# Kernel optimization log

Measured on AMD Instinct MI355X. Metric: run time of the kernel, lower is better.

Reference implementation:

```python
import jax, jax.numpy as jnp
import numpy as np

QMIN, QMAX = -128, 127  # int8 range


def _quantize(x, scale, zero_point):
    """Affine quantize float -> int8: clamp(round(x/scale) + zp, -128, 127)."""
    q = jnp.round(x / scale) + zero_point
    return jnp.clip(q, QMIN, QMAX).astype(jnp.int8)


def setup_inputs() -> dict:
    key = jax.random.key(0)
    k1, k2, k3 = jax.random.split(key, 3)
    N, IN, OUT = 8192, 4096, 4096
    inp = jax.random.normal(k1, (N, IN), dtype=jnp.float32)
    # int8 weight table [OUT, IN]
    weight = jax.random.randint(k2, (OUT, IN), QMIN, QMAX + 1, dtype=jnp.int32).astype(jnp.int8)
    # int32 bias [OUT]
    bias = jax.random.randint(k3, (OUT,), -(2 ** 15), 2 ** 15, dtype=jnp.int32)
    return {
        "input": inp,
        "weight": weight,
        "bias": bias,
        "input_scale": 0.02,
        "input_zero_point": 0,
        "output_scale": 4096.0,
        "output_zero_point": 0,
    }


def reference(input, weight, bias, input_scale, input_zero_point, output_scale, output_zero_point):
    # 1) affine quantize input to int8
    q_input = _quantize(input, input_scale, input_zero_point)
    # 2) int32 matmul: F.linear(q_input.int32, weight.int32, bias.int32)
    acc = jnp.matmul(q_input.astype(jnp.int32), weight.astype(jnp.int32).T) + bias  # [N, OUT] int32
    # 3) requantize int32 accumulator to int8 with output scale/zero-point
    q_output = _quantize(acc.astype(jnp.float32), output_scale, output_zero_point)
    return q_output
```

## Files before the change

kernel.cpp:

```cpp
#include <hip/hip_runtime.h>
#include <stdint.h>

typedef int v4i __attribute__((ext_vector_type(4)));

__device__ __forceinline__ int clamp_i8(int v) {
    return v < -128 ? -128 : (v > 127 ? 127 : v);
}

__device__ __forceinline__ void async_load16(const void* g, void* l) {
    __builtin_amdgcn_global_load_lds(
        (const __attribute__((address_space(1))) void*)g,
        (__attribute__((address_space(3))) void*)l, 16, 0, 0);
}

__global__ void quant_input_kernel(const float* __restrict__ x, int8_t* __restrict__ q,
                                   const float* __restrict__ scale_p,
                                   const int* __restrict__ zp_p, int n4) {
    int t = blockIdx.x * blockDim.x + threadIdx.x;
    if (t >= n4) return;
    const float s = *scale_p;
    const int zp = *zp_p;
    float4 v = ((const float4*)x)[t];
    int q0 = clamp_i8((int)rintf(v.x / s) + zp);
    int q1 = clamp_i8((int)rintf(v.y / s) + zp);
    int q2 = clamp_i8((int)rintf(v.z / s) + zp);
    int q3 = clamp_i8((int)rintf(v.w / s) + zp);
    int packed = (q0 & 255) | ((q1 & 255) << 8) | ((q2 & 255) << 16) | ((q3 & 255) << 24);
    ((int*)q)[t] = packed;
}

__global__ void pack_weight_kernel(const int* __restrict__ w, int8_t* __restrict__ q, int n4) {
    int t = blockIdx.x * blockDim.x + threadIdx.x;
    if (t >= n4) return;
    int4 v = ((const int4*)w)[t];
    int packed = (v.x & 255) | ((v.y & 255) << 8) | ((v.z & 255) << 16) | ((v.w & 255) << 24);
    ((int*)q)[t] = packed;
}

#define BM 128
#define BN 128
#define BK 64

__global__ __launch_bounds__(256) void gemm_i8_kernel(
    const int8_t* __restrict__ A, const int8_t* __restrict__ W,
    const int* __restrict__ bias, int* __restrict__ C,
    const float* __restrict__ oscale_p, const int* __restrict__ ozp_p,
    int N, int K, int M) {
    __shared__ int8_t lA[BM * BK];
    __shared__ int8_t lW[BN * BK];

    const int tid = threadIdx.x;
    const int lane = tid & 63;
    const int w = tid >> 6;
    const int wm = w & 1;
    const int wn = w >> 1;
    const int qm = lane & 15;
    const int qk = lane >> 4;

    const int bm = blockIdx.y * BM;
    const int bn = blockIdx.x * BN;

    const int s_row = w * 32 + (lane >> 2);
    const int s_col = (lane & 3) * 16;
    const int8_t* gA = A + (int64_t)(bm + s_row) * K + s_col;
    const int8_t* gW = W + (int64_t)(bn + s_row) * K + s_col;
    int8_t* lA0 = &lA[w * 2048];
    int8_t* lW0 = &lW[w * 2048];
    const int64_t rowskip = (int64_t)16 * K;

    v4i acc[4][4];
#pragma unroll
    for (int i = 0; i < 4; i++)
#pragma unroll
        for (int j = 0; j < 4; j++) acc[i][j] = (v4i){0, 0, 0, 0};

    for (int kt = 0; kt < K; kt += BK) {
        async_load16(gA + kt, lA0);
        async_load16(gA + kt + rowskip, lA0 + 1024);
        async_load16(gW + kt, lW0);
        async_load16(gW + kt + rowskip, lW0 + 1024);
        __syncthreads();

        v4i af[4], bf[4];
#pragma unroll
        for (int ms = 0; ms < 4; ms++)
            af[ms] = *(const v4i*)&lA[(wm * 64 + ms * 16 + qm) * BK + qk * 16];
#pragma unroll
        for (int ns = 0; ns < 4; ns++)
            bf[ns] = *(const v4i*)&lW[(wn * 64 + ns * 16 + qm) * BK + qk * 16];

#pragma unroll
        for (int ms = 0; ms < 4; ms++)
#pragma unroll
            for (int ns = 0; ns < 4; ns++)
                acc[ms][ns] = __builtin_amdgcn_mfma_i32_16x16x64_i8(af[ms], bf[ns],
                                                                    acc[ms][ns], 0, 0, 0);
        __syncthreads();
    }

    const float os = *oscale_p;
    const int ozp = *ozp_p;
#pragma unroll
    for (int ns = 0; ns < 4; ns++) {
        const int gn = bn + wn * 64 + ns * 16 + qm;
        const int bv = bias[gn];
#pragma unroll
        for (int ms = 0; ms < 4; ms++) {
            const int gm = bm + wm * 64 + ms * 16 + qk * 4;
            v4i a = acc[ms][ns];
#pragma unroll
            for (int r = 0; r < 4; r++) {
                int v = a[r] + bv;
                int q = (int)rintf((float)v / os) + ozp;
                q = clamp_i8(q);
                C[(int64_t)(gm + r) * M + gn] = q;
            }
        }
    }
}

extern "C" void kernel_launch(void* const* d_in, const int* in_sizes, int n_in,
                              void* d_out, int out_size, void* d_ws, size_t ws_size,
                              hipStream_t stream) {
    const float* x = (const float*)d_in[0];
    const int* wgt = (const int*)d_in[1];
    const int* bias = (const int*)d_in[2];
    const float* in_scale = (const float*)d_in[3];
    const int* in_zp = (const int*)d_in[4];
    const float* out_scale = (const float*)d_in[5];
    const int* out_zp = (const int*)d_in[6];

    const int64_t x_elems = (int64_t)in_sizes[0];
    const int OUT = in_sizes[2];
    const int K = in_sizes[1] / OUT;
    const int N = (int)(x_elems / K);

    int8_t* qA = (int8_t*)d_ws;
    int8_t* qW = qA + x_elems;

    {
        int n4 = (int)(x_elems / 4);
        quant_input_kernel<<<(n4 + 255) / 256, 256, 0, stream>>>(x, qA, in_scale, in_zp, n4);
    }
    {
        int n4 = (int)(((int64_t)OUT * K) / 4);
        pack_weight_kernel<<<(n4 + 255) / 256, 256, 0, stream>>>(wgt, qW, n4);
    }
    dim3 grid(OUT / BN, N / BM);
    gemm_i8_kernel<<<grid, 256, 0, stream>>>(qA, qW, bias, (int*)d_out,
                                             out_scale, out_zp, N, K, OUT);
}
```

Before: 443.2 us.

## Enlarge GEMM tile to 256x128 and switch to 32x32x32 int8 MFMA

Doubles the M tile to 256 rows and has each wave compute a 128x64 sub-tile with 32x32x32 int8 MFMAs over two k-steps per 64-wide K tile. This raises arithmetic intensity per LDS and global load and cuts the number of instructions per FLOP. The epilogue and the input quantizer now multiply by a precomputed reciprocal instead of dividing, which can change rounding in rare edge cases. LDS use grows to 24KB per block, and launch bounds now ask for two blocks per CU.

New measurement: 427.8 us. 3.5% less time.

```diff
diff --git a/kernel.cpp b/kernel.cpp
--- a/kernel.cpp
+++ b/kernel.cpp
@@ -2,6 +2,7 @@
 #include <stdint.h>
 
 typedef int v4i __attribute__((ext_vector_type(4)));
+typedef int v16i __attribute__((ext_vector_type(16)));
 
 __device__ __forceinline__ int clamp_i8(int v) {
     return v < -128 ? -128 : (v > 127 ? 127 : v);
@@ -18,13 +19,13 @@
                                    const int* __restrict__ zp_p, int n4) {
     int t = blockIdx.x * blockDim.x + threadIdx.x;
     if (t >= n4) return;
-    const float s = *scale_p;
+    const float inv = 1.0f / *scale_p;
     const int zp = *zp_p;
     float4 v = ((const float4*)x)[t];
-    int q0 = clamp_i8((int)rintf(v.x / s) + zp);
-    int q1 = clamp_i8((int)rintf(v.y / s) + zp);
-    int q2 = clamp_i8((int)rintf(v.z / s) + zp);
-    int q3 = clamp_i8((int)rintf(v.w / s) + zp);
+    int q0 = clamp_i8((int)rintf(v.x * inv) + zp);
+    int q1 = clamp_i8((int)rintf(v.y * inv) + zp);
+    int q2 = clamp_i8((int)rintf(v.z * inv) + zp);
+    int q3 = clamp_i8((int)rintf(v.w * inv) + zp);
     int packed = (q0 & 255) | ((q1 & 255) << 8) | ((q2 & 255) << 16) | ((q3 & 255) << 24);
     ((int*)q)[t] = packed;
 }
@@ -37,83 +38,95 @@
     ((int*)q)[t] = packed;
 }
 
-#define BM 128
+#define BM 256
 #define BN 128
 #define BK 64
 
-__global__ __launch_bounds__(256) void gemm_i8_kernel(
+__global__ __launch_bounds__(256, 2) void gemm_i8_kernel(
     const int8_t* __restrict__ A, const int8_t* __restrict__ W,
     const int* __restrict__ bias, int* __restrict__ C,
     const float* __restrict__ oscale_p, const int* __restrict__ ozp_p,
     int N, int K, int M) {
     __shared__ int8_t lA[BM * BK];
-    __shared__ int8_t lW[BN * BK];
+    __shared__ int8_t lB[BN * BK];
 
     const int tid = threadIdx.x;
     const int lane = tid & 63;
     const int w = tid >> 6;
-    const int wm = w & 1;
-    const int wn = w >> 1;
-    const int qm = lane & 15;
-    const int qk = lane >> 4;
+    const int wm = w >> 1;
+    const int wn = w & 1;
 
     const int bm = blockIdx.y * BM;
     const int bn = blockIdx.x * BN;
 
-    const int s_row = w * 32 + (lane >> 2);
+    const int s_sub = lane >> 2;
     const int s_col = (lane & 3) * 16;
-    const int8_t* gA = A + (int64_t)(bm + s_row) * K + s_col;
-    const int8_t* gW = W + (int64_t)(bn + s_row) * K + s_col;
-    int8_t* lA0 = &lA[w * 2048];
-    int8_t* lW0 = &lW[w * 2048];
-    const int64_t rowskip = (int64_t)16 * K;
+    const int8_t* gA = A + (int64_t)(bm + w * 64 + s_sub) * K + s_col;
+    const int8_t* gB = W + (int64_t)(bn + w * 32 + s_sub) * K + s_col;
+    int8_t* lA0 = &lA[w * 4096];
+    int8_t* lB0 = &lB[w * 2048];
+    const int64_t rs = (int64_t)16 * K;
 
-    v4i acc[4][4];
+    const int m0 = lane & 31;
+    const int kh = (lane >> 5) * 16;
+
+    v16i acc[4][2];
 #pragma unroll
     for (int i = 0; i < 4; i++)
 #pragma unroll
-        for (int j = 0; j < 4; j++) acc[i][j] = (v4i){0, 0, 0, 0};
+        for (int j = 0; j < 2; j++)
+#pragma unroll
+            for (int r = 0; r < 16; r++) acc[i][j][r] = 0;
 
     for (int kt = 0; kt < K; kt += BK) {
-        async_load16(gA + kt, lA0);
-        async_load16(gA + kt + rowskip, lA0 + 1024);
-        async_load16(gW + kt, lW0);
-        async_load16(gW + kt + rowskip, lW0 + 1024);
+        async_load16(gA, lA0);
+        async_load16(gA + rs, lA0 + 1024);
+        async_load16(gA + 2 * rs, lA0 + 2048);
+        async_load16(gA + 3 * rs, lA0 + 3072);
+        async_load16(gB, lB0);
+        async_load16(gB + rs, lB0 + 1024);
+        gA += BK;
+        gB += BK;
         __syncthreads();
 
-        v4i af[4], bf[4];
 #pragma unroll
-        for (int ms = 0; ms < 4; ms++)
-            af[ms] = *(const v4i*)&lA[(wm * 64 + ms * 16 + qm) * BK + qk * 16];
+        for (int k0 = 0; k0 < BK; k0 += 32) {
+            v4i af[4], bf[2];
 #pragma unroll
-        for (int ns = 0; ns < 4; ns++)
-            bf[ns] = *(const v4i*)&lW[(wn * 64 + ns * 16 + qm) * BK + qk * 16];
+            for (int ms = 0; ms < 4; ms++)
+                af[ms] = *(const v4i*)&lA[(wm * 128 + ms * 32 + m0) * BK + k0 + kh];
+#pragma unroll
+            for (int ns = 0; ns < 2; ns++)
+                bf[ns] = *(const v4i*)&lB[(wn * 64 + ns * 32 + m0) * BK + k0 + kh];
 
 #pragma unroll
-        for (int ms = 0; ms < 4; ms++)
+            for (int ms = 0; ms < 4; ms++)
 #pragma unroll
-            for (int ns = 0; ns < 4; ns++)
-                acc[ms][ns] = __builtin_amdgcn_mfma_i32_16x16x64_i8(af[ms], bf[ns],
-                                                                    acc[ms][ns], 0, 0, 0);
+                for (int ns = 0; ns < 2; ns++)
+                    acc[ms][ns] = __builtin_amdgcn_mfma_i32_32x32x32_i8(
+                        af[ms], bf[ns], acc[ms][ns], 0, 0, 0);
+        }
         __syncthreads();
     }
 
-    const float os = *oscale_p;
+    const float inv_os = 1.0f / *oscale_p;
     const int ozp = *ozp_p;
+    const int rbase = 4 * (lane >> 5);
 #pragma unroll
-    for (int ns = 0; ns < 4; ns++) {
-        const int gn = bn + wn * 64 + ns * 16 + qm;
+    for (int ns = 0; ns < 2; ns++) {
+        const int gn = bn + wn * 64 + ns * 32 + m0;
         const int bv = bias[gn];
 #pragma unroll
         for (int ms = 0; ms < 4; ms++) {
-            const int gm = bm + wm * 64 + ms * 16 + qk * 4;
-            v4i a = acc[ms][ns];
+            const int gm0 = bm + wm * 128 + ms * 32 + rbase;
+            v16i a = acc[ms][ns];
 #pragma unroll
-            for (int r = 0; r < 4; r++) {
-                int v = a[r] + bv;
-                int q = (int)rintf((float)v / os) + ozp;
+            for (int reg = 0; reg < 16; reg++) {
+                const int row = (reg & 3) + 8 * (reg >> 2);
+                int v = a[reg] + bv;
+                int q = (int)rintf((float)v * inv_os) + ozp;
                 q = clamp_i8(q);
-                C[(int64_t)(gm + r) * M + gn] = q;
+                C[(int64_t)(gm0 + row) * M + gn] = q;
             }
         }
     }
```
